# Kernel optimization log

Hardware: AMD Instinct MI355X
Metric: run time of the kernel (lower is better)

Reference implementation:

```python
import jax, jax.numpy as jnp
import numpy as np

EPS = 1e-5  # BatchNorm1d default eps


def _xavier_uniform(key, shape):
    # torch xavier: fan_in = shape[1]*prod(shape[2:]), fan_out = shape[0]*prod(shape[2:])
    rf = int(np.prod(shape[2:])) if len(shape) > 2 else 1
    fan_in = shape[1] * rf
    fan_out = shape[0] * rf
    bound = float(np.sqrt(6.0 / (fan_in + fan_out)))
    return jax.random.uniform(key, shape, jnp.float32, -bound, bound)


def setup_inputs() -> dict:
    key = jax.random.key(0)
    ks = jax.random.split(key, 6)
    d_in, h1, h2, d_out = 256, 512, 512, 256
    B = 4096
    x = jax.random.normal(ks[0], (B, 1, d_in), dtype=jnp.float32)
    W1 = _xavier_uniform(ks[1], (h1, d_in))
    b1 = jnp.zeros((h1,), jnp.float32)
    gamma = jnp.ones((1, 1, 1), jnp.float32)   # BatchNorm1d(1) weight
    beta = jnp.zeros((1, 1, 1), jnp.float32)   # BatchNorm1d(1) bias
    coeffs2 = _xavier_uniform(ks[2], (2, h2, h1, 16))
    bias2 = jnp.zeros((1, h2), jnp.float32)
    coeffs3 = _xavier_uniform(ks[3], (2, d_out, h2, 8))
    bias3 = jnp.zeros((1, d_out), jnp.float32)
    return {"x": x, "W1": W1, "b1": b1, "gamma": gamma, "beta": beta,
            "coeffs2": coeffs2, "bias2": bias2, "coeffs3": coeffs3, "bias3": bias3}


def _fourier_kan(x, coeffs, bias, gridsize):
    # x: (N, in)  coeffs: (2, out, in, grid)  ->  (N, out)
    k = jnp.arange(1, gridsize + 1, dtype=x.dtype)          # (grid,)
    arg = x[:, :, None] * k                                  # (N, in, grid) -- basis computed ONCE
    y = jnp.einsum('nig,oig->no', jnp.cos(arg), coeffs[0])
    y = y + jnp.einsum('nig,oig->no', jnp.sin(arg), coeffs[1])
    return y + bias


def reference(x, W1, b1, gamma, beta, coeffs2, bias2, coeffs3, bias3):
    # x: (B, 1, d_in)
    h = jnp.einsum('bcd,hd->bch', x, W1) + b1                # Linear -> (B,1,h1)
    # BatchNorm1d(1), training-mode batch stats over (N, L) for the single channel
    mean = jnp.mean(h, axis=(0, 2), keepdims=True)
    var = jnp.mean((h - mean) ** 2, axis=(0, 2), keepdims=True)
    h = gamma * (h - mean) * jax.lax.rsqrt(var + EPS) + beta
    h = jax.nn.relu(h)
    h = h.reshape(-1, h.shape[-1])                           # (B, h1)
    h = _fourier_kan(h, coeffs2, bias2, 16)                  # (B, h2)
    h = _fourier_kan(h, coeffs3, bias3, 8)                   # (B, out)
    return jax.nn.softmax(h, axis=1)
```

## Files before the change

kernel.cpp:

```cpp
#include <hip/hip_runtime.h>
#include <hip/hip_fp16.h>
#include <stdint.h>

typedef unsigned short u16;
typedef unsigned int u32;
typedef long i64;
typedef short bf16x8 __attribute__((ext_vector_type(8)));
typedef float f32x4 __attribute__((ext_vector_type(4)));

#define SCALE_C   1024.f
#define INV_SCALE 0.0009765625f

__device__ __forceinline__ float bf2f(u16 v) { return __uint_as_float(((u32)v) << 16); }

__device__ __forceinline__ u16 f2bf(float a) {
  u32 u = __float_as_uint(a); u += 0x7FFFu + ((u >> 16) & 1u); return (u16)(u >> 16);
}

__device__ __forceinline__ u32 packbf2(float a, float b) {
  u32 ua = __float_as_uint(a); ua += 0x7FFFu + ((ua >> 16) & 1u);
  u32 ub = __float_as_uint(b); ub += 0x7FFFu + ((ub >> 16) & 1u);
  return (ua >> 16) | (ub & 0xFFFF0000u);
}

__device__ __forceinline__ u32 packfp8x4(float a, float b, float c, float d) {
  u32 lo = (u32)__builtin_amdgcn_cvt_pk_fp8_f32(a, b, 0, false);
  return (u32)__builtin_amdgcn_cvt_pk_fp8_f32(c, d, (int)lo, true);
}

__device__ __forceinline__ float inval(const void* p, int idx, int isf) {
  return isf ? ((const float*)p)[idx] : bf2f(((const u16*)p)[idx]);
}

__device__ __forceinline__ void async_cp16(const void* g, void* l) {
  __builtin_amdgcn_global_load_lds(
      (const __attribute__((address_space(1))) void*)g,
      (__attribute__((address_space(3))) void*)l, 16, 0, 0);
}

__device__ __forceinline__ void basis16(float a, u32* pk) {
  float s1, c1; __sincosf(a, &s1, &c1);
  float t2 = c1 + c1;
  float cg[16], sg[16];
  cg[0] = c1; sg[0] = s1;
  cg[1] = fmaf(t2, c1, -1.f); sg[1] = t2 * s1;
  #pragma unroll
  for (int g = 2; g < 16; ++g) {
    cg[g] = fmaf(t2, cg[g-1], -cg[g-2]);
    sg[g] = fmaf(t2, sg[g-1], -sg[g-2]);
  }
  #pragma unroll
  for (int j = 0; j < 4; ++j) pk[j]   = packfp8x4(cg[4*j], cg[4*j+1], cg[4*j+2], cg[4*j+3]);
  #pragma unroll
  for (int j = 0; j < 4; ++j) pk[4+j] = packfp8x4(sg[4*j], sg[4*j+1], sg[4*j+2], sg[4*j+3]);
}

__device__ __forceinline__ void split_body(
    const void* __restrict__ src, u16* __restrict__ dst, int i, int isf, int lo_pos)
{
  int row = i >> 6, g = i & 63;
  float v[4];
  if (isf) {
    float4 t = ((const float4*)src)[i];
    v[0] = t.x; v[1] = t.y; v[2] = t.z; v[3] = t.w;
  } else {
    uint2 t = ((const uint2*)src)[i];
    const u16* p = (const u16*)&t;
    v[0] = bf2f(p[0]); v[1] = bf2f(p[1]); v[2] = bf2f(p[2]); v[3] = bf2f(p[3]);
  }
  u16 hi[4]; float lo[4];
  #pragma unroll
  for (int j = 0; j < 4; ++j) { hi[j] = f2bf(v[j]); lo[j] = v[j] - bf2f(hi[j]); }
  u32 hw0 = (u32)hi[0] | ((u32)hi[1] << 16);
  u32 hw1 = (u32)hi[2] | ((u32)hi[3] << 16);
  u32 lw0 = packbf2(lo[0], lo[1]);
  u32 lw1 = packbf2(lo[2], lo[3]);
  u32* base = (u32*)(dst + (size_t)row * 768);
  int c = g * 2;
  base[c] = hw0; base[c + 1] = hw1;
  if (lo_pos == 1) {
    base[128 + c] = lw0; base[128 + c + 1] = lw1;
    base[256 + c] = hw0; base[256 + c + 1] = hw1;
  } else {
    base[128 + c] = hw0; base[128 + c + 1] = hw1;
    base[256 + c] = lw0; base[256 + c + 1] = lw1;
  }
}

__global__ __launch_bounds__(256) void prep_all_kernel(
    const void* __restrict__ x, const void* __restrict__ W1,
    u16* __restrict__ Xs, u16* __restrict__ W1s,
    const void* __restrict__ c2, unsigned char* __restrict__ w2f8,
    const void* __restrict__ c3, unsigned char* __restrict__ w3f8,
    int* __restrict__ flag)
{
  __shared__ int sf[4];
  const int t = threadIdx.x, wave = t >> 6;
  {
    float v = fabsf(bf2f(((const u16*)W1)[t & 127]));
    int bad = !(v < 1e6f);
    unsigned long long b = __ballot(bad);
    if ((t & 63) == 0) sf[wave] = (b != 0ull) ? 1 : 0;
  }
  __syncthreads();
  const int isf = sf[0] | sf[1] | sf[2] | sf[3];
  const int bid = blockIdx.x;
  if (bid == 0 && t == 0) *flag = isf;
  if (bid < 1024) {
    split_body(x, Xs, bid * 256 + t, isf, 1);
  } else if (bid < 1152) {
    split_body(W1, W1s, (bid - 1024) * 256 + t, isf, 2);
  } else if (bid < 2176) {
    int u = (bid - 1152) * 256 + t;
    int o = u >> 9, i = u & 511;
    u32* d = (u32*)(w2f8 + (size_t)o * 16384 + i * 32);
    if (isf) {
      const float4* f0 = (const float4*)((const float*)c2 + ((size_t)o * 512 + i) * 16);
      const float4* f1 = (const float4*)((const float*)c2 + (size_t)512 * 512 * 16 + ((size_t)o * 512 + i) * 16);
      #pragma unroll
      for (int j = 0; j < 4; ++j) { float4 v = f0[j]; d[j]   = packfp8x4(v.x*SCALE_C, v.y*SCALE_C, v.z*SCALE_C, v.w*SCALE_C); }
      #pragma unroll
      for (int j = 0; j < 4; ++j) { float4 v = f1[j]; d[4+j] = packfp8x4(v.x*SCALE_C, v.y*SCALE_C, v.z*SCALE_C, v.w*SCALE_C); }
    } else {
      const u16* s0 = (const u16*)c2 + ((size_t)o * 512 + i) * 16;
      const u16* s1 = (const u16*)c2 + (size_t)512 * 512 * 16 + ((size_t)o * 512 + i) * 16;
      #pragma unroll
      for (int j = 0; j < 4; ++j) d[j]   = packfp8x4(bf2f(s0[4*j])*SCALE_C, bf2f(s0[4*j+1])*SCALE_C, bf2f(s0[4*j+2])*SCALE_C, bf2f(s0[4*j+3])*SCALE_C);
      #pragma unroll
      for (int j = 0; j < 4; ++j) d[4+j] = packfp8x4(bf2f(s1[4*j])*SCALE_C, bf2f(s1[4*j+1])*SCALE_C, bf2f(s1[4*j+2])*SCALE_C, bf2f(s1[4*j+3])*SCALE_C);
    }
  } else {
    int u = (bid - 2176) * 256 + t;
    int o = u >> 9, i = u & 511;
    u32* d = (u32*)(w3f8 + (size_t)o * 8192 + i * 16);
    if (isf) {
      const float4* f0 = (const float4*)((const float*)c3 + ((size_t)o * 512 + i) * 8);
      const float4* f1 = (const float4*)((const float*)c3 + (size_t)256 * 512 * 8 + ((size_t)o * 512 + i) * 8);
      #pragma unroll
      for (int j = 0; j < 2; ++j) { float4 v = f0[j]; d[j]   = packfp8x4(v.x*SCALE_C, v.y*SCALE_C, v.z*SCALE_C, v.w*SCALE_C); }
      #pragma unroll
      for (int j = 0; j < 2; ++j) { float4 v = f1[j]; d[2+j] = packfp8x4(v.x*SCALE_C, v.y*SCALE_C, v.z*SCALE_C, v.w*SCALE_C); }
    } else {
      const u16* s0 = (const u16*)c3 + ((size_t)o * 512 + i) * 8;
      const u16* s1 = (const u16*)c3 + (size_t)256 * 512 * 8 + ((size_t)o * 512 + i) * 8;
      #pragma unroll
      for (int j = 0; j < 2; ++j) d[j]   = packfp8x4(bf2f(s0[4*j])*SCALE_C, bf2f(s0[4*j+1])*SCALE_C, bf2f(s0[4*j+2])*SCALE_C, bf2f(s0[4*j+3])*SCALE_C);
      #pragma unroll
      for (int j = 0; j < 2; ++j) d[2+j] = packfp8x4(bf2f(s1[4*j])*SCALE_C, bf2f(s1[4*j+1])*SCALE_C, bf2f(s1[4*j+2])*SCALE_C, bf2f(s1[4*j+3])*SCALE_C);
    }
  }
}

#define L1_LD 136
__global__ __launch_bounds__(256) void l1_kernel(
    const u16* __restrict__ xs, const u16* __restrict__ w1s, const void* __restrict__ b1,
    const int* __restrict__ flag, float* __restrict__ H, float2* __restrict__ PT)
{
  __shared__ u16 sA[64 * L1_LD];
  __shared__ u16 sB[64 * L1_LD];
  __shared__ float redbuf[8];
  const int n0 = blockIdx.x * 64, o0 = blockIdx.y * 64;
  const int t = threadIdx.x, wave = t >> 6, lane = t & 63, quad = lane >> 4, l16 = lane & 15;
  const int isf = *flag;
  f32x4 acc[4] = {};
  for (int ks = 0; ks < 768; ks += 128) {
    #pragma unroll
    for (int r = 0; r < 4; ++r) {
      int idx = t + r * 256, row = idx >> 4, col = idx & 15;
      *(uint4*)&sA[row * L1_LD + col * 8] =
          *((const uint4*)(xs + (size_t)(n0 + row) * 768 + ks) + col);
    }
    #pragma unroll
    for (int r = 0; r < 4; ++r) {
      int idx = t + r * 256, row = idx >> 4, col = idx & 15;
      *(uint4*)&sB[row * L1_LD + col * 8] =
          *((const uint4*)(w1s + (size_t)(o0 + row) * 768 + ks) + col);
    }
    __syncthreads();
    #pragma unroll
    for (int kk = 0; kk < 128; kk += 32) {
      bf16x8 av = *(const bf16x8*)&sA[(wave * 16 + l16) * L1_LD + kk + quad * 8];
      #pragma unroll
      for (int fo = 0; fo < 4; ++fo) {
        bf16x8 bv = *(const bf16x8*)&sB[(fo * 16 + l16) * L1_LD + kk + quad * 8];
        acc[fo] = __builtin_amdgcn_mfma_f32_16x16x32_bf16(av, bv, acc[fo], 0, 0, 0);
      }
    }
    __syncthreads();
  }
  float s = 0.f, sq = 0.f;
  #pragma unroll
  for (int fo = 0; fo < 4; ++fo) {
    int o = o0 + fo * 16 + l16;
    float bias = inval(b1, o, isf);
    #pragma unroll
    for (int r = 0; r < 4; ++r) {
      int n = n0 + wave * 16 + quad * 4 + r;
      float h = acc[fo][r] + bias;
      H[(size_t)n * 512 + o] = h;
      s += h; sq += h * h;
    }
  }
  #pragma unroll
  for (int off = 32; off; off >>= 1) { s += __shfl_down(s, off); sq += __shfl_down(sq, off); }
  if (lane == 0) { redbuf[wave] = s; redbuf[4 + wave] = sq; }
  __syncthreads();
  if (t == 0) {
    float S = redbuf[0] + redbuf[1] + redbuf[2] + redbuf[3];
    float Q = redbuf[4] + redbuf[5] + redbuf[6] + redbuf[7];
    PT[blockIdx.y * 64 + blockIdx.x] = make_float2(S, Q);
  }
}

#define K2_LDB 128
__global__ __launch_bounds__(256) void kan2_kernel(
    const float* __restrict__ H, const unsigned char* __restrict__ w2f8,
    const void* __restrict__ gammap, const void* __restrict__ betap,
    const int* __restrict__ flag, const float2* __restrict__ PT,
    float* __restrict__ P, int kzT)
{
  __shared__ unsigned char sA8[2][64 * K2_LDB];
  __shared__ unsigned char sB8[2][128 * K2_LDB];
  __shared__ float sred[8];
  const int n0 = blockIdx.x * 64, o0 = blockIdx.y * 128, kz = blockIdx.z;
  const int t = threadIdx.x, wave = t >> 6, lane = t & 63, quad = lane >> 4, l16 = lane & 15;
  const int wm = (wave & 1) * 32, wo = (wave >> 1) * 64;
  const int isf = *flag;
  const int am = t >> 2, ai = t & 3;
  const int q = 128 / kzT, rr = 128 % kzT;
  const int nst = q + (kz < rr ? 1 : 0);
  const int i0 = (kz * q + (kz < rr ? kz : rr)) * 4;
  const int r0 = t >> 3, seg = t & 7;
  const unsigned char* bsrc = w2f8 + (size_t)(o0 + r0) * 16384 + (size_t)i0 * 32
                              + ((seg * 16) ^ ((r0 & 7) << 4));
  const float* hsrc = H + (size_t)(n0 + am) * 512 + i0 + ai;
  const int ldsOff = wave * 8 * K2_LDB;
  #pragma unroll
  for (int p = 0; p < 4; ++p)
    async_cp16(bsrc + (size_t)p * 32 * 16384, &sB8[0][ldsOff + p * 32 * K2_LDB]);
  bsrc += 128;
  float ph = *hsrc; hsrc += 4;
  {
    float2 pa = PT[t], pb = PT[t + 256];
    float ss = pa.x + pb.x, qs = pa.y + pb.y;
    #pragma unroll
    for (int off = 32; off; off >>= 1) { ss += __shfl_down(ss, off); qs += __shfl_down(qs, off); }
    if (lane == 0) { sred[wave] = ss; sred[4 + wave] = qs; }
  }
  __syncthreads();
  const float Ssum = sred[0] + sred[1] + sred[2] + sred[3];
  const float Qsum = sred[4] + sred[5] + sred[6] + sred[7];
  const float Nn = 4096.f * 512.f;
  const float mean = Ssum / Nn;
  const float rstd = rsqrtf(Qsum / Nn - mean * mean + 1e-5f);
  const float gs = inval(gammap, 0, isf) * rstd;
  const float beta = inval(betap, 0, isf);
  const int acol0 = (ai * 32) ^ ((am & 7) << 4);
  const int acol1 = (ai * 32 + 16) ^ ((am & 7) << 4);
  const int csw = (l16 & 7) << 4;
  f32x4 acc[2][4] = {};
  u32 pk[8];
  {
    float a = fmaxf((ph - mean) * gs + beta, 0.f);
    basis16(a, pk);
  }
  if (nst > 1) { ph = *hsrc; hsrc += 4; }
  *(uint4*)&sA8[0][am * K2_LDB + acol0] = *(uint4*)&pk[0];
  *(uint4*)&sA8[0][am * K2_LDB + acol1] = *(uint4*)&pk[4];
  __syncthreads();
  int cur = 0;
  for (int s = 0; s < nst; ++s) {
    const int nxt = cur ^ 1;
    if (s + 1 < nst) {
      #pragma unroll
      for (int p = 0; p < 4; ++p)
        async_cp16(bsrc + (size_t)p * 32 * 16384, &sB8[nxt][ldsOff + p * 32 * K2_LDB]);
      bsrc += 128;
      float a = fmaxf((ph - mean) * gs + beta, 0.f);
      basis16(a, pk);
      if (s + 2 < nst) { ph = *hsrc; hsrc += 4; }
    }
    #pragma unroll
    for (int kk = 0; kk < 128; kk += 32) {
      const int cb = (kk + quad * 8) ^ csw;
      i64 bfr[4], afr[2];
      #pragma unroll
      for (int fo = 0; fo < 4; ++fo)
        bfr[fo] = *(const i64*)&sB8[cur][(wo + fo * 16 + l16) * K2_LDB + cb];
      #pragma unroll
      for (int fm = 0; fm < 2; ++fm)
        afr[fm] = *(const i64*)&sA8[cur][(wm + fm * 16 + l16) * K2_LDB + cb];
      #pragma unroll
      for (int fm = 0; fm < 2; ++fm)
      #pragma unroll
      for (int fo = 0; fo < 4; ++fo)
        acc[fm][fo] = __builtin_amdgcn_mfma_f32_16x16x32_fp8_fp8(afr[fm], bfr[fo], acc[fm][fo], 0, 0, 0);
    }
    if (s + 1 < nst) {
      *(uint4*)&sA8[nxt][am * K2_LDB + acol0] = *(uint4*)&pk[0];
      *(uint4*)&sA8[nxt][am * K2_LDB + acol1] = *(uint4*)&pk[4];
    }
    __syncthreads();
    cur = nxt;
  }
  float* Pk = P + (size_t)kz * (4096 * 512);
  #pragma unroll
  for (int fm = 0; fm < 2; ++fm)
  #pragma unroll
  for (int fo = 0; fo < 4; ++fo) {
    int o = o0 + wo + fo * 16 + l16;
    #pragma unroll
    for (int r = 0; r < 4; ++r) {
      int n = n0 + wm + fm * 16 + quad * 4 + r;
      Pk[(size_t)n * 512 + o] = acc[fm][fo][r] * INV_SCALE;
    }
  }
}

#define K3_LDB 128
__global__ __launch_bounds__(256) void kan3_kernel(
    const float* __restrict__ P2, const void* __restrict__ bias2,
    const unsigned char* __restrict__ w3f8,
    const int* __restrict__ flag, float* __restrict__ Q, int kzT2)
{
  __shared__ unsigned char sA8[32 * K3_LDB];
  __shared__ unsigned char sB8[256 * K3_LDB];
  const int n0 = blockIdx.x * 32, kz = blockIdx.z;
  const int t = threadIdx.x, wave = t >> 6, lane = t & 63, quad = lane >> 4, l16 = lane & 15;
  const int wo = wave * 64;
  const int am = t >> 3, ai = t & 7;
  const int nst = 10 + (kz < 4 ? 1 : 0);
  const int i0 = (kz * 10 + (kz < 4 ? kz : 4)) * 8;
  const int r0 = t >> 3, seg = t & 7;
  const int isf = *flag;
  const unsigned char* bsrc = w3f8 + (size_t)r0 * 8192 + (size_t)i0 * 16
                              + ((seg * 16) ^ ((r0 & 7) << 4));
  const float* psrc = P2 + (size_t)(n0 + am) * 512 + i0 + ai;
  unsigned char* ldsB = &sB8[wave * 8 * K3_LDB];
  const int acol = (ai * 16) ^ ((am & 7) << 4);
  const int csw  = (l16 & 7) << 4;
  f32x4 acc[2][4] = {};
  #pragma unroll
  for (int p = 0; p < 8; ++p)
    async_cp16(bsrc + (size_t)p * 32 * 8192, ldsB + p * 32 * K3_LDB);
  float ph;
  {
    float v = inval(bias2, i0 + ai, isf);
    for (int k = 0; k < kzT2; ++k) v += psrc[(size_t)k * 4096 * 512];
    ph = v;
  }
  for (int s = 0; s < nst; ++s) {
    {
      float s1, c1; __sincosf(ph, &s1, &c1);
      float t2 = c1 + c1;
      float cg[8], sg[8];
      cg[0] = c1; sg[0] = s1;
      cg[1] = fmaf(t2, c1, -1.f); sg[1] = t2 * s1;
      #pragma unroll
      for (int g = 2; g < 8; ++g) {
        cg[g] = fmaf(t2, cg[g-1], -cg[g-2]);
        sg[g] = fmaf(t2, sg[g-1], -sg[g-2]);
      }
      u32 pk[4];
      pk[0] = packfp8x4(cg[0], cg[1], cg[2], cg[3]);
      pk[1] = packfp8x4(cg[4], cg[5], cg[6], cg[7]);
      pk[2] = packfp8x4(sg[0], sg[1], sg[2], sg[3]);
      pk[3] = packfp8x4(sg[4], sg[5], sg[6], sg[7]);
      *(uint4*)&sA8[am * K3_LDB + acol] = *(uint4*)&pk[0];
    }
    __syncthreads();
    psrc += 8;
    if (s + 1 < nst) {
      float v = inval(bias2, i0 + (s + 1) * 8 + ai, isf);
      for (int k = 0; k < kzT2; ++k) v += psrc[(size_t)k * 4096 * 512];
      ph = v;
    }
    #pragma unroll
    for (int kk = 0; kk < 128; kk += 32) {
      const int cb = (kk + quad * 8) ^ csw;
      i64 bfr[4], afr[2];
      #pragma unroll
      for (int fo = 0; fo < 4; ++fo)
        bfr[fo] = *(const i64*)&sB8[(wo + fo * 16 + l16) * K3_LDB + cb];
      #pragma unroll
      for (int fm = 0; fm < 2; ++fm)
        afr[fm] = *(const i64*)&sA8[(fm * 16 + l16) * K3_LDB + cb];
      #pragma unroll
      for (int fm = 0; fm < 2; ++fm)
      #pragma unroll
      for (int fo = 0; fo < 4; ++fo)
        acc[fm][fo] = __builtin_amdgcn_mfma_f32_16x16x32_fp8_fp8(afr[fm], bfr[fo], acc[fm][fo], 0, 0, 0);
    }
    __syncthreads();
    bsrc += 128;
    if (s + 1 < nst) {
      #pragma unroll
      for (int p = 0; p < 8; ++p)
        async_cp16(bsrc + (size_t)p * 32 * 8192, ldsB + p * 32 * K3_LDB);
    }
  }
  float* Qk = Q + (size_t)kz * (4096 * 256);
  #pragma unroll
  for (int fm = 0; fm < 2; ++fm)
  #pragma unroll
  for (int fo = 0; fo < 4; ++fo) {
    int o = wo + fo * 16 + l16;
    #pragma unroll
    for (int r = 0; r < 4; ++r) {
      int n = n0 + fm * 16 + quad * 4 + r;
      Qk[(size_t)n * 256 + o] = acc[fm][fo][r] * INV_SCALE;
    }
  }
}

__global__ __launch_bounds__(256) void softmax_kernel(
    const float* __restrict__ Q, const void* __restrict__ bias3,
    const int* __restrict__ flag, float* __restrict__ out)
{
  const int t = threadIdx.x, wave = t >> 6, lane = t & 63;
  const int row = blockIdx.x * 4 + wave;
  const int isf = *flag;
  size_t base = (size_t)row * 256 + lane * 4;
  float v0 = 0.f, v1 = 0.f, v2 = 0.f, v3 = 0.f;
  #pragma unroll
  for (int k = 0; k < 6; ++k) {
    float4 a = *(const float4*)(Q + (size_t)k * 4096 * 256 + base);
    v0 += a.x; v1 += a.y; v2 += a.z; v3 += a.w;
  }
  int o = lane * 4;
  v0 += inval(bias3, o + 0, isf);
  v1 += inval(bias3, o + 1, isf);
  v2 += inval(bias3, o + 2, isf);
  v3 += inval(bias3, o + 3, isf);
  float m = fmaxf(fmaxf(v0, v1), fmaxf(v2, v3));
  #pragma unroll
  for (int off = 32; off; off >>= 1) m = fmaxf(m, __shfl_xor(m, off));
  float e0 = __expf(v0 - m), e1 = __expf(v1 - m), e2 = __expf(v2 - m), e3 = __expf(v3 - m);
  float s = e0 + e1 + e2 + e3;
  #pragma unroll
  for (int off = 32; off; off >>= 1) s += __shfl_xor(s, off);
  float inv = 1.f / s;
  *(float4*)(out + base) = make_float4(e0 * inv, e1 * inv, e2 * inv, e3 * inv);
}

extern "C" void kernel_launch(void* const* d_in, const int* in_sizes, int n_in,
                              void* d_out, int out_size, void* d_ws, size_t ws_size,
                              hipStream_t stream)
{
  const void* x     = d_in[0];
  const void* W1    = d_in[1];
  const void* b1    = d_in[2];
  const void* gamma = d_in[3];
  const void* beta  = d_in[4];
  const void* c2    = d_in[5];
  const void* bias2 = d_in[6];
  const void* c3    = d_in[7];
  const void* bias3 = d_in[8];

  const int kz2 = 3;

  char* ws = (char*)d_ws;
  float*          H    = (float*)(ws + 0);
  unsigned char*  W2F8 = (unsigned char*)(ws + (16ull << 20));
  unsigned char*  W3F8 = (unsigned char*)(ws + (24ull << 20));
  u16*            Xs   = (u16*)(ws + (26ull << 20));
  u16*            W1s  = (u16*)(ws + (33ull << 20));
  float*          P2   = (float*)(ws + (34ull << 20));
  float*          Q3   = (float*)(ws + 0);
  size_t tail = (34ull << 20) + (size_t)kz2 * (8ull << 20) + 524288;
  float2* PT   = (float2*)(ws + tail);
  int*    FLAG = (int*)   (ws + tail + 65536);

  prep_all_kernel<<<dim3(2688), dim3(256), 0, stream>>>(x, W1, Xs, W1s, c2, W2F8, c3, W3F8, FLAG);
  l1_kernel   <<<dim3(64, 8), dim3(256), 0, stream>>>(Xs, W1s, b1, FLAG, H, PT);
  kan2_kernel <<<dim3(64, 4, kz2), dim3(256), 0, stream>>>(H, W2F8, gamma, beta, FLAG, PT, P2, kz2);
  kan3_kernel <<<dim3(128, 1, 6), dim3(256), 0, stream>>>(P2, bias2, W3F8, FLAG, Q3, kz2);
  softmax_kernel<<<dim3(1024), dim3(256), 0, stream>>>(Q3, bias3, FLAG, (float*)d_out);
}
```

Baseline: 214.2 us.

## Warp-specialize kan2 into producer and MFMA consumer waves with wider output tiles

The kan2 kernel now runs 512-thread blocks. Four producer waves issue the async FP8 weight copies, compute the BatchNorm+ReLU Fourier basis and write the next A tile. Four consumer waves only run MFMAs on a 64x256 output tile, using double-buffered shared memory of 80KB. The split-K factor goes from 3 to 4, so each split covers an even share of stages and the grid is re-laid out to match. The aim is to hide load and basis-computation latency behind the MFMAs. The cost is that half the waves never issue MFMAs, per-wave accumulator registers grow, and an extra partial-sum buffer must be written and later read.

```diff
diff --git a/kernel.cpp b/kernel.cpp
--- a/kernel.cpp
+++ b/kernel.cpp
@@ -213,106 +213,115 @@
 }
 
 #define K2_LDB 128
-__global__ __launch_bounds__(256) void kan2_kernel(
+__global__ __launch_bounds__(512, 4) void kan2_kernel(
     const float* __restrict__ H, const unsigned char* __restrict__ w2f8,
     const void* __restrict__ gammap, const void* __restrict__ betap,
     const int* __restrict__ flag, const float2* __restrict__ PT,
     float* __restrict__ P, int kzT)
 {
-  __shared__ unsigned char sA8[2][64 * K2_LDB];
-  __shared__ unsigned char sB8[2][128 * K2_LDB];
-  __shared__ float sred[8];
-  const int n0 = blockIdx.x * 64, o0 = blockIdx.y * 128, kz = blockIdx.z;
+  __shared__ __attribute__((aligned(16))) unsigned char smem[81920];
+  float* sred = (float*)(smem + 81888);
+  const int n0 = blockIdx.x * 64, o0 = blockIdx.y * 256, kz = blockIdx.z;
   const int t = threadIdx.x, wave = t >> 6, lane = t & 63, quad = lane >> 4, l16 = lane & 15;
-  const int wm = (wave & 1) * 32, wo = (wave >> 1) * 64;
+  const int nst = 128 / kzT;
+  const int i0 = kz * nst * 4;
+  const int csw = (l16 & 7) << 4;
   const int isf = *flag;
-  const int am = t >> 2, ai = t & 3;
-  const int q = 128 / kzT, rr = 128 % kzT;
-  const int nst = q + (kz < rr ? 1 : 0);
-  const int i0 = (kz * q + (kz < rr ? kz : rr)) * 4;
-  const int r0 = t >> 3, seg = t & 7;
-  const unsigned char* bsrc = w2f8 + (size_t)(o0 + r0) * 16384 + (size_t)i0 * 32
-                              + ((seg * 16) ^ ((r0 & 7) << 4));
-  const float* hsrc = H + (size_t)(n0 + am) * 512 + i0 + ai;
-  const int ldsOff = wave * 8 * K2_LDB;
-  #pragma unroll
-  for (int p = 0; p < 4; ++p)
-    async_cp16(bsrc + (size_t)p * 32 * 16384, &sB8[0][ldsOff + p * 32 * K2_LDB]);
-  bsrc += 128;
-  float ph = *hsrc; hsrc += 4;
-  {
-    float2 pa = PT[t], pb = PT[t + 256];
+
+  const int pt = t - 256;
+  const int am = pt >> 2, ai = pt & 3;
+  const int r0 = pt >> 3, seg = pt & 7;
+  const unsigned char* bsrc = w2f8 + (size_t)(o0 + (r0 & 63)) * 16384 + (size_t)i0 * 32
+                              + (((seg & 7) * 16) ^ ((r0 & 7) << 4));
+  const float* hsrc = H + (size_t)(n0 + (am & 63)) * 512 + i0 + (ai & 3);
+  const int acol0 = ((ai & 3) * 32) ^ ((am & 7) << 4);
+  const int acol1 = ((ai & 3) * 32 + 16) ^ ((am & 7) << 4);
+  float mean = 0.f, gs = 0.f, beta = 0.f, ph = 0.f;
+  u32 pk[8];
+
+  if (wave >= 4) {
+    unsigned char* b0 = smem + 16384 + (wave - 4) * 1024;
+    #pragma unroll
+    for (int p = 0; p < 8; ++p)
+      async_cp16(bsrc + (size_t)p * 32 * 16384, b0 + p * 4096);
+    float2 pa = PT[pt], pb = PT[pt + 256];
     float ss = pa.x + pb.x, qs = pa.y + pb.y;
     #pragma unroll
     for (int off = 32; off; off >>= 1) { ss += __shfl_down(ss, off); qs += __shfl_down(qs, off); }
-    if (lane == 0) { sred[wave] = ss; sred[4 + wave] = qs; }
+    if (lane == 0) { sred[(wave - 4) * 2] = ss; sred[(wave - 4) * 2 + 1] = qs; }
   }
   __syncthreads();
-  const float Ssum = sred[0] + sred[1] + sred[2] + sred[3];
-  const float Qsum = sred[4] + sred[5] + sred[6] + sred[7];
-  const float Nn = 4096.f * 512.f;
-  const float mean = Ssum / Nn;
-  const float rstd = rsqrtf(Qsum / Nn - mean * mean + 1e-5f);
-  const float gs = inval(gammap, 0, isf) * rstd;
-  const float beta = inval(betap, 0, isf);
-  const int acol0 = (ai * 32) ^ ((am & 7) << 4);
-  const int acol1 = (ai * 32 + 16) ^ ((am & 7) << 4);
-  const int csw = (l16 & 7) << 4;
-  f32x4 acc[2][4] = {};
-  u32 pk[8];
-  {
-    float a = fmaxf((ph - mean) * gs + beta, 0.f);
+  if (wave >= 4) {
+    const float Ssum = sred[0] + sred[2] + sred[4] + sred[6];
+    const float Qsum = sred[1] + sred[3] + sred[5] + sred[7];
+    const float Nn = 4096.f * 512.f;
+    mean = Ssum / Nn;
+    const float rstd = rsqrtf(Qsum / Nn - mean * mean + 1e-5f);
+    gs = inval(gammap, 0, isf) * rstd;
+    beta = inval(betap, 0, isf);
+    float a = fmaxf((*hsrc - mean) * gs + beta, 0.f);
+    hsrc += 4;
     basis16(a, pk);
-  }
-  if (nst > 1) { ph = *hsrc; hsrc += 4; }
-  *(uint4*)&sA8[0][am * K2_LDB + acol0] = *(uint4*)&pk[0];
-  *(uint4*)&sA8[0][am * K2_LDB + acol1] = *(uint4*)&pk[4];
+    *(uint4*)&smem[am * K2_LDB + acol0] = *(uint4*)&pk[0];
+    *(uint4*)&smem[am * K2_LDB + acol1] = *(uint4*)&pk[4];
+    if (nst > 1) { ph = *hsrc; hsrc += 4; }
+  }
   __syncthreads();
+
+  f32x4 acc[2][8] = {};
+  const int wm = (wave & 1) * 32, wo = (wave >> 1) * 128;
   int cur = 0;
   for (int s = 0; s < nst; ++s) {
     const int nxt = cur ^ 1;
-    if (s + 1 < nst) {
-      #pragma unroll
-      for (int p = 0; p < 4; ++p)
-        async_cp16(bsrc + (size_t)p * 32 * 16384, &sB8[nxt][ldsOff + p * 32 * K2_LDB]);
-      bsrc += 128;
-      float a = fmaxf((ph - mean) * gs + beta, 0.f);
-      basis16(a, pk);
-      if (s + 2 < nst) { ph = *hsrc; hsrc += 4; }
-    }
-    #pragma unroll
-    for (int kk = 0; kk < 128; kk += 32) {
-      const int cb = (kk + quad * 8) ^ csw;
-      i64 bfr[4], afr[2];
-      #pragma unroll
-      for (int fo = 0; fo < 4; ++fo)
-        bfr[fo] = *(const i64*)&sB8[cur][(wo + fo * 16 + l16) * K2_LDB + cb];
-      #pragma unroll
-      for (int fm = 0; fm < 2; ++fm)
-        afr[fm] = *(const i64*)&sA8[cur][(wm + fm * 16 + l16) * K2_LDB + cb];
-      #pragma unroll
-      for (int fm = 0; fm < 2; ++fm)
-      #pragma unroll
-      for (int fo = 0; fo < 4; ++fo)
-        acc[fm][fo] = __builtin_amdgcn_mfma_f32_16x16x32_fp8_fp8(afr[fm], bfr[fo], acc[fm][fo], 0, 0, 0);
-    }
-    if (s + 1 < nst) {
-      *(uint4*)&sA8[nxt][am * K2_LDB + acol0] = *(uint4*)&pk[0];
-      *(uint4*)&sA8[nxt][am * K2_LDB + acol1] = *(uint4*)&pk[4];
+    if (wave >= 4) {
+      if (s + 1 < nst) {
+        bsrc += 128;
+        unsigned char* bn = smem + 16384 + nxt * 32768 + (wave - 4) * 1024;
+        #pragma unroll
+        for (int p = 0; p < 8; ++p)
+          async_cp16(bsrc + (size_t)p * 32 * 16384, bn + p * 4096);
+        float a = fmaxf((ph - mean) * gs + beta, 0.f);
+        basis16(a, pk);
+        unsigned char* an = smem + nxt * 8192;
+        *(uint4*)&an[am * K2_LDB + acol0] = *(uint4*)&pk[0];
+        *(uint4*)&an[am * K2_LDB + acol1] = *(uint4*)&pk[4];
+        if (s + 2 < nst) { ph = *hsrc; hsrc += 4; }
+      }
+    } else {
+      const unsigned char* ac = smem + cur * 8192;
+      const unsigned char* bc = smem + 16384 + cur * 32768;
+      #pragma unroll
+      for (int kk = 0; kk < 128; kk += 32) {
+        const int cb = (kk + quad * 8) ^ csw;
+        i64 bfr[8], afr[2];
+        #pragma unroll
+        for (int fo = 0; fo < 8; ++fo)
+          bfr[fo] = *(const i64*)&bc[(wo + fo * 16 + l16) * K2_LDB + cb];
+        #pragma unroll
+        for (int fm = 0; fm < 2; ++fm)
+          afr[fm] = *(const i64*)&ac[(wm + fm * 16 + l16) * K2_LDB + cb];
+        #pragma unroll
+        for (int fm = 0; fm < 2; ++fm)
+        #pragma unroll
+        for (int fo = 0; fo < 8; ++fo)
+          acc[fm][fo] = __builtin_amdgcn_mfma_f32_16x16x32_fp8_fp8(afr[fm], bfr[fo], acc[fm][fo], 0, 0, 0);
+      }
     }
     __syncthreads();
     cur = nxt;
   }
-  float* Pk = P + (size_t)kz * (4096 * 512);
-  #pragma unroll
-  for (int fm = 0; fm < 2; ++fm)
-  #pragma unroll
-  for (int fo = 0; fo < 4; ++fo) {
-    int o = o0 + wo + fo * 16 + l16;
-    #pragma unroll
-    for (int r = 0; r < 4; ++r) {
-      int n = n0 + wm + fm * 16 + quad * 4 + r;
-      Pk[(size_t)n * 512 + o] = acc[fm][fo][r] * INV_SCALE;
+  if (wave < 4) {
+    float* Pk = P + (size_t)kz * (4096 * 512);
+    #pragma unroll
+    for (int fm = 0; fm < 2; ++fm)
+    #pragma unroll
+    for (int fo = 0; fo < 8; ++fo) {
+      int o = o0 + wo + fo * 16 + l16;
+      #pragma unroll
+      for (int r = 0; r < 4; ++r) {
+        int n = n0 + wm + fm * 16 + quad * 4 + r;
+        Pk[(size_t)n * 512 + o] = acc[fm][fo][r] * INV_SCALE;
+      }
     }
   }
 }
@@ -457,7 +466,7 @@
   const void* c3    = d_in[7];
   const void* bias3 = d_in[8];
 
-  const int kz2 = 3;
+  const int kz2 = 4;
 
   char* ws = (char*)d_ws;
   float*          H    = (float*)(ws + 0);
@@ -473,7 +482,7 @@
 
   prep_all_kernel<<<dim3(2688), dim3(256), 0, stream>>>(x, W1, Xs, W1s, c2, W2F8, c3, W3F8, FLAG);
   l1_kernel   <<<dim3(64, 8), dim3(256), 0, stream>>>(Xs, W1s, b1, FLAG, H, PT);
-  kan2_kernel <<<dim3(64, 4, kz2), dim3(256), 0, stream>>>(H, W2F8, gamma, beta, FLAG, PT, P2, kz2);
+  kan2_kernel <<<dim3(64, 2, kz2), dim3(512), 0, stream>>>(H, W2F8, gamma, beta, FLAG, PT, P2, kz2);
   kan3_kernel <<<dim3(128, 1, 6), dim3(256), 0, stream>>>(P2, bias2, W3F8, FLAG, Q3, kz2);
   softmax_kernel<<<dim3(1024), dim3(256), 0, stream>>>(Q3, bias3, FLAG, (float*)d_out);
 }
```

Result: faster. 198.7 us (-7.2%).
